# Performance work log

Hardware: AMD Instinct MI355X
Metric: run time of the kernel (lower is better)

The kernel has to match this reference:

```python
import jax, jax.numpy as jnp
import numpy as np

N_NODES = 100000
N_EDGES = 1600000
D = 128
BN_EPS = 1e-5

def setup_inputs() -> dict:
    key = jax.random.key(0)
    ks = jax.random.split(key, 6)
    h = jax.random.normal(ks[0], (N_NODES, D), dtype=jnp.float32)
    src = jax.random.randint(ks[1], (N_EDGES,), 0, N_NODES, dtype=jnp.int32)
    dst = jax.random.randint(ks[2], (N_EDGES,), 0, N_NODES, dtype=jnp.int32)
    eps = jnp.zeros((1,), dtype=jnp.float32)
    # 2-layer GIN apply_func MLP, scaled for stable activations
    W1 = jax.random.normal(ks[3], (D, D), dtype=jnp.float32) / np.sqrt(D)
    b1 = jnp.zeros((D,), dtype=jnp.float32)
    W2 = jax.random.normal(ks[4], (D, D), dtype=jnp.float32) / np.sqrt(D)
    b2 = jnp.zeros((D,), dtype=jnp.float32)
    gamma = jnp.ones((D,), dtype=jnp.float32)
    beta = jnp.zeros((D,), dtype=jnp.float32)
    return {"h": h, "src": src, "dst": dst, "eps": eps,
            "W1": W1, "b1": b1, "W2": W2, "b2": b2,
            "gamma": gamma, "beta": beta}

def reference(h, src, dst, eps, W1, b1, W2, b2, gamma, beta):
    # --- neighbor sum aggregation: update_all(copy_u('h'), fn.sum) ---
    msgs = h[src]                                   # [E, D] irregular gather
    neigh = jax.ops.segment_sum(msgs, dst, num_segments=N_NODES)  # [N, D]
    # --- eps-scaled self term ---
    x = (1.0 + eps[0]) * h + neigh                  # [N, D]
    # --- apply_func: 2-layer MLP ---
    x = jax.nn.relu(x @ W1 + b1)
    x = x @ W2 + b2
    # --- BatchNorm1d over node dim (training-mode batch stats) ---
    mean = jnp.mean(x, axis=0)
    var = jnp.mean(jnp.square(x - mean), axis=0)
    x = (x - mean) * jax.lax.rsqrt(var + BN_EPS) * gamma + beta
    # --- activation + residual ---
    x = jax.nn.relu(x)
    x = h + x  # residual (in_dim == out_dim)
    return x
```

## Files before the change

### kernel.cpp

```cpp
#include <hip/hip_runtime.h>

#define NN 100000
#define NE 1600000
#define DD 128
#define BN_EPS 1e-5f

#define SBSH 9
#define SBSZ 512
#define NSB ((NN + SBSZ - 1) / SBSZ)
#define CAPS 9216
#define EPB 8192
#define NBLK ((NE + EPB - 1) / EPB)
#define PREPBLKS 828
#define GRID_PS (NBLK + PREPBLKS)
#define TSZ 64
#define NTILE ((NN + TSZ - 1) / TSZ)
#define BN_BLOCKS 1024

typedef __attribute__((ext_vector_type(8))) short short8;
typedef __attribute__((ext_vector_type(4))) float floatx4;

__device__ __forceinline__ unsigned short f2bf(float f) {
    union { float f; unsigned u; } v; v.f = f;
    return (unsigned short)((v.u + 0x7FFFu + ((v.u >> 16) & 1u)) >> 16);
}
__device__ __forceinline__ float bf2f(unsigned short u) {
    union { unsigned u; float f; } v; v.u = ((unsigned)u) << 16;
    return v.f;
}

__global__ __launch_bounds__(256) void prep_scatter_kernel(
    const float* __restrict__ W1, const float* __restrict__ W2,
    unsigned short* __restrict__ W1t, unsigned short* __restrict__ W2t,
    const float* __restrict__ h, unsigned short* __restrict__ hb, int do_hb,
    const int* __restrict__ src, const int* __restrict__ dst,
    int* __restrict__ scnt, int* __restrict__ sbuf)
{
    __shared__ int bins[256];
    __shared__ int lofs[256];
    __shared__ int gbase[256];
    __shared__ int stmp[256];
    __shared__ int sorted[EPB];
    int t = threadIdx.x;

    if (blockIdx.x < NBLK) {
        bins[t] = 0;
        __syncthreads();
        int base = blockIdx.x * EPB;
        int ecnt = min(EPB, NE - base);
        for (int i = t; i < ecnt; i += 256)
            atomicAdd(&bins[dst[base + i] >> SBSH], 1);
        __syncthreads();
        int c = bins[t];
        stmp[t] = c;
        __syncthreads();
#pragma unroll
        for (int ofs = 1; ofs < 256; ofs <<= 1) {
            int u = (t >= ofs) ? stmp[t - ofs] : 0;
            __syncthreads();
            stmp[t] += u;
            __syncthreads();
        }
        int excl = stmp[t] - c;
        lofs[t] = excl;
        int gb = (t < NSB && c) ? atomicAdd(&scnt[t], c) : 0;
        gbase[t] = t * CAPS + gb;
        bins[t] = excl;
        __syncthreads();

        for (int i = t; i < ecnt; i += 256) {
            int d = dst[base + i];
            int p = atomicAdd(&bins[d >> SBSH], 1);
            sorted[p] = (src[base + i] << SBSH) | (d & (SBSZ - 1));
        }
        __syncthreads();

        for (int sb = t; sb < NSB; sb += 256) {
            int lb = lofs[sb], le = bins[sb];
            int g = gbase[sb];
            for (int j = lb; j < le; ++j)
                sbuf[g + (j - lb)] = sorted[j];
        }
    } else {
        int tid0 = (blockIdx.x - NBLK) * 256 + t;
        int stride = PREPBLKS * 256;
        for (int i = tid0; i < DD * DD; i += stride) {
            int n = i >> 7, k = i & 127;
            W1t[i] = f2bf(W1[k * DD + n]);
            W2t[i] = f2bf(W2[k * DD + n]);
        }
        if (do_hb) {
            const float4* h4 = (const float4*)h;
            ushort4* hb4 = (ushort4*)hb;
            for (int i = tid0; i < NN * (DD / 4); i += stride) {
                float4 v = h4[i];
                ushort4 o;
                o.x = f2bf(v.x); o.y = f2bf(v.y); o.z = f2bf(v.z); o.w = f2bf(v.w);
                hb4[i] = o;
            }
        }
    }
}

__global__ __launch_bounds__(512) void permute_kernel(
    const int* __restrict__ scnt, int* __restrict__ sbuf,
    int2* __restrict__ off2)
{
    __shared__ int ew[CAPS];
    __shared__ int cnt[SBSZ];
    __shared__ int beg[SBSZ];
    __shared__ int cur[SBSZ];
    __shared__ int stmp[512];
    int sb = blockIdx.x, t = threadIdx.x;
    cnt[t] = 0;
    __syncthreads();
    int n = min(scnt[sb], CAPS);
    int sbase = sb * CAPS;
    for (int i = t; i < n; i += 512) {
        int e = sbuf[sbase + i];
        ew[i] = e;
        atomicAdd(&cnt[e & (SBSZ - 1)], 1);
    }
    __syncthreads();
    int c = cnt[t];
    stmp[t] = c;
    __syncthreads();
#pragma unroll
    for (int ofs = 1; ofs < 512; ofs <<= 1) {
        int u = (t >= ofs) ? stmp[t - ofs] : 0;
        __syncthreads();
        stmp[t] += u;
        __syncthreads();
    }
    int excl = stmp[t] - c;
    beg[t] = excl;
    cur[t] = excl;
    off2[sb * SBSZ + t] = make_int2(sbase + excl, sbase + excl + c);
    __syncthreads();
    for (int i = t; i < n; i += 512) {
        int e = ew[i];
        int p = atomicAdd(&cur[e & (SBSZ - 1)], 1);
        sbuf[sbase + p] = e >> SBSH;
    }
}

template <bool HB>
__global__ __launch_bounds__(256) void gather_mlp_kernel(
    const float* __restrict__ h, const unsigned short* __restrict__ hb,
    const float* __restrict__ eps, const int2* __restrict__ off2,
    const int* __restrict__ srcs,
    const unsigned short* __restrict__ W1t, const unsigned short* __restrict__ W2t,
    const float* __restrict__ b1, const float* __restrict__ b2,
    unsigned short* __restrict__ Y, float* __restrict__ stats)
{
    __shared__ __align__(16) unsigned short xl[TSZ * 136];
    __shared__ __align__(16) char un[17408];

    int* beg64 = (int*)un;
    int* cnt64 = (int*)(un + 256);
    int* dh    = (int*)(un + 512);
    int* dcur  = (int*)(un + 768);
    unsigned char* order = (unsigned char*)(un + 1024);
    unsigned short* wl = (unsigned short*)un;
    float* sred = (float*)un;
    float* qred = sred + 2048;

    const int b = blockIdx.x;
    const int t = threadIdx.x;
    const int lane = t & 63;
    const int wv = t >> 6;
    const int m = lane & 15;
    const int hi = lane >> 4;

    if (t < 64) dh[t] = 0;
    __syncthreads();
    if (t < 64) {
        int2 oo = off2[b * TSZ + t];
        beg64[t] = oo.x;
        cnt64[t] = oo.y - oo.x;
        atomicAdd(&dh[min(cnt64[t], 63)], 1);
    }
    __syncthreads();
    if (t < 64) dcur[t] = dh[t];
    __syncthreads();
#pragma unroll
    for (int ofs = 1; ofs < 64; ofs <<= 1) {
        int u = (t < 64 && t >= ofs) ? dcur[t - ofs] : 0;
        __syncthreads();
        if (t < 64) dcur[t] += u;
        __syncthreads();
    }
    if (t < 64) dcur[t] -= dh[t];
    __syncthreads();
    if (t < 64) {
        int p = atomicAdd(&dcur[min(cnt64[t], 63)], 1);
        order[p] = (unsigned char)t;
    }
    __syncthreads();

    const float sE = 1.0f + eps[0];
    const float4* h4 = (const float4*)h;
    const short8* hb8 = (const short8*)hb;
    const int c8 = t & 15;
#pragma unroll
    for (int pass = 0; pass < 4; ++pass) {
        int nl = order[pass * 16 + (t >> 4)];
        int node = b * TSZ + nl;
        if (node >= NN) {
            short8 z = {0, 0, 0, 0, 0, 0, 0, 0};
            *(short8*)&xl[nl * 136 + c8 * 8] = z;
            continue;
        }
        float4 a0 = h4[node * 32 + c8 * 2];
        float4 a1 = h4[node * 32 + c8 * 2 + 1];
        float acc[8] = {sE * a0.x, sE * a0.y, sE * a0.z, sE * a0.w,
                        sE * a1.x, sE * a1.y, sE * a1.z, sE * a1.w};
        int e = beg64[nl], eend = beg64[nl] + cnt64[nl];
        if (HB) {
            for (; e + 3 < eend; e += 4) {
                int s0 = srcs[e], s1 = srcs[e + 1], s2 = srcs[e + 2], s3 = srcs[e + 3];
                short8 v0 = hb8[s0 * 16 + c8];
                short8 v1 = hb8[s1 * 16 + c8];
                short8 v2 = hb8[s2 * 16 + c8];
                short8 v3 = hb8[s3 * 16 + c8];
#pragma unroll
                for (int j = 0; j < 8; ++j) {
                    float t0 = bf2f((unsigned short)v0[j]) + bf2f((unsigned short)v1[j]);
                    float t1 = bf2f((unsigned short)v2[j]) + bf2f((unsigned short)v3[j]);
                    acc[j] += t0 + t1;
                }
            }
            for (; e < eend; ++e) {
                short8 v0 = hb8[srcs[e] * 16 + c8];
#pragma unroll
                for (int j = 0; j < 8; ++j) acc[j] += bf2f((unsigned short)v0[j]);
            }
        } else {
            for (; e + 1 < eend; e += 2) {
                int s0 = srcs[e], s1 = srcs[e + 1];
                float4 u0 = h4[s0 * 32 + c8 * 2], u1 = h4[s0 * 32 + c8 * 2 + 1];
                float4 w0 = h4[s1 * 32 + c8 * 2], w1 = h4[s1 * 32 + c8 * 2 + 1];
                acc[0] += u0.x + w0.x; acc[1] += u0.y + w0.y;
                acc[2] += u0.z + w0.z; acc[3] += u0.w + w0.w;
                acc[4] += u1.x + w1.x; acc[5] += u1.y + w1.y;
                acc[6] += u1.z + w1.z; acc[7] += u1.w + w1.w;
            }
            if (e < eend) {
                int s0 = srcs[e];
                float4 u0 = h4[s0 * 32 + c8 * 2], u1 = h4[s0 * 32 + c8 * 2 + 1];
                acc[0] += u0.x; acc[1] += u0.y; acc[2] += u0.z; acc[3] += u0.w;
                acc[4] += u1.x; acc[5] += u1.y; acc[6] += u1.z; acc[7] += u1.w;
            }
        }
        short8 o;
#pragma unroll
        for (int j = 0; j < 8; ++j) o[j] = (short)f2bf(acc[j]);
        *(short8*)&xl[nl * 136 + c8 * 8] = o;
    }
    __syncthreads();

    floatx4 acc[8];
#pragma unroll
    for (int i = 0; i < 8; ++i) acc[i] = (floatx4){0.f, 0.f, 0.f, 0.f};
    const short8* W1t8 = (const short8*)W1t;
#pragma unroll
    for (int hh = 0; hh < 2; ++hh) {
#pragma unroll
        for (int l = 0; l < 4; ++l) {
            int idx = t + l * 256;
            int nr = idx >> 4, c = idx & 15;
            *(short8*)&wl[nr * 136 + c * 8] = W1t8[(hh * 64 + nr) * 16 + c];
        }
        __syncthreads();
#pragma unroll
        for (int kc = 0; kc < 4; ++kc) {
            short8 a = *(const short8*)&xl[(wv * 16 + m) * 136 + kc * 32 + hi * 8];
#pragma unroll
            for (int ntl = 0; ntl < 4; ++ntl) {
                short8 bb = *(const short8*)&wl[(ntl * 16 + m) * 136 + kc * 32 + hi * 8];
                acc[hh * 4 + ntl] =
                    __builtin_amdgcn_mfma_f32_16x16x32_bf16(a, bb, acc[hh * 4 + ntl], 0, 0, 0);
            }
        }
        __syncthreads();
    }
#pragma unroll
    for (int nt = 0; nt < 8; ++nt) {
        float bv = b1[nt * 16 + m];
#pragma unroll
        for (int r = 0; r < 4; ++r) {
            float v = fmaxf(acc[nt][r] + bv, 0.f);
            xl[(wv * 16 + hi * 4 + r) * 136 + nt * 16 + m] = f2bf(v);
        }
    }
    __syncthreads();

#pragma unroll
    for (int i = 0; i < 8; ++i) acc[i] = (floatx4){0.f, 0.f, 0.f, 0.f};
    const short8* W2t8 = (const short8*)W2t;
#pragma unroll
    for (int hh = 0; hh < 2; ++hh) {
#pragma unroll
        for (int l = 0; l < 4; ++l) {
            int idx = t + l * 256;
            int nr = idx >> 4, c = idx & 15;
            *(short8*)&wl[nr * 136 + c * 8] = W2t8[(hh * 64 + nr) * 16 + c];
        }
        __syncthreads();
#pragma unroll
        for (int kc = 0; kc < 4; ++kc) {
            short8 a = *(const short8*)&xl[(wv * 16 + m) * 136 + kc * 32 + hi * 8];
#pragma unroll
            for (int ntl = 0; ntl < 4; ++ntl) {
                short8 bb = *(const short8*)&wl[(ntl * 16 + m) * 136 + kc * 32 + hi * 8];
                acc[hh * 4 + ntl] =
                    __builtin_amdgcn_mfma_f32_16x16x32_bf16(a, bb, acc[hh * 4 + ntl], 0, 0, 0);
            }
        }
        __syncthreads();
    }

#pragma unroll
    for (int nt = 0; nt < 8; ++nt) {
        float bv = b2[nt * 16 + m];
        float ss = 0.f, qq = 0.f;
#pragma unroll
        for (int r = 0; r < 4; ++r) {
            int row = wv * 16 + hi * 4 + r;
            float v = acc[nt][r] + bv;
            xl[row * 136 + nt * 16 + m] = f2bf(v);
            if (b * TSZ + row < NN) { ss += v; qq += v * v; }
        }
        sred[(nt * 16 + m) * 16 + wv * 4 + hi] = ss;
        qred[(nt * 16 + m) * 16 + wv * 4 + hi] = qq;
    }
    __syncthreads();

#pragma unroll
    for (int l = 0; l < 4; ++l) {
        int idx = t + l * 256;
        int row = idx >> 4, c = idx & 15;
        int g = b * TSZ + row;
        if (g < NN)
            ((short8*)Y)[g * 16 + c] = *(const short8*)&xl[row * 136 + c * 8];
    }
    if (t < 128) {
        float s = 0.f, q = 0.f;
#pragma unroll
        for (int j = 0; j < 16; ++j) { s += sred[t * 16 + j]; q += qred[t * 16 + j]; }
        atomicAdd(&stats[t], s);
        atomicAdd(&stats[DD + t], q);
    }
}

__global__ __launch_bounds__(256) void bn_final_kernel(
    const unsigned short* __restrict__ Y, const float* __restrict__ h,
    const float* __restrict__ gamma, const float* __restrict__ beta,
    const float* __restrict__ stats, float* __restrict__ out)
{
    const float invN = 1.0f / (float)NN;
    int t0 = blockIdx.x * 256 + threadIdx.x;
    int c8 = t0 & 15;
    float sc[8], sh[8];
#pragma unroll
    for (int j = 0; j < 8; ++j) {
        int col = c8 * 8 + j;
        float mu = stats[col] * invN;
        float var = stats[DD + col] * invN - mu * mu;
        float s = rsqrtf(var + BN_EPS) * gamma[col];
        sc[j] = s;
        sh[j] = beta[col] - mu * s;
    }
    const short8* Y8 = (const short8*)Y;
    const float4* H4 = (const float4*)h;
    float4* O4 = (float4*)out;
    const int total = NN * 16;
    const int stride = BN_BLOCKS * 256;
    for (int i = t0; i < total; i += stride) {
        short8 u = Y8[i];
        float4 h0 = H4[2 * i], h1 = H4[2 * i + 1];
        float4 r0, r1;
        r0.x = h0.x + fmaxf(bf2f((unsigned short)u[0]) * sc[0] + sh[0], 0.f);
        r0.y = h0.y + fmaxf(bf2f((unsigned short)u[1]) * sc[1] + sh[1], 0.f);
        r0.z = h0.z + fmaxf(bf2f((unsigned short)u[2]) * sc[2] + sh[2], 0.f);
        r0.w = h0.w + fmaxf(bf2f((unsigned short)u[3]) * sc[3] + sh[3], 0.f);
        r1.x = h1.x + fmaxf(bf2f((unsigned short)u[4]) * sc[4] + sh[4], 0.f);
        r1.y = h1.y + fmaxf(bf2f((unsigned short)u[5]) * sc[5] + sh[5], 0.f);
        r1.z = h1.z + fmaxf(bf2f((unsigned short)u[6]) * sc[6] + sh[6], 0.f);
        r1.w = h1.w + fmaxf(bf2f((unsigned short)u[7]) * sc[7] + sh[7], 0.f);
        O4[2 * i] = r0;
        O4[2 * i + 1] = r1;
    }
}

extern "C" void kernel_launch(void* const* d_in, const int* in_sizes, int n_in,
                              void* d_out, int out_size, void* d_ws, size_t ws_size,
                              hipStream_t stream)
{
    const float* h     = (const float*)d_in[0];
    const int*   src   = (const int*)d_in[1];
    const int*   dst   = (const int*)d_in[2];
    const float* eps   = (const float*)d_in[3];
    const float* W1    = (const float*)d_in[4];
    const float* b1    = (const float*)d_in[5];
    const float* W2    = (const float*)d_in[6];
    const float* b2    = (const float*)d_in[7];
    const float* gamma = (const float*)d_in[8];
    const float* beta  = (const float*)d_in[9];
    float* out = (float*)d_out;

    char* w = (char*)d_ws;
    size_t o = 0;
    float* stats    = (float*)(w + o); o += 256 * 4;
    int* scnt       = (int*)(w + o); o += 256 * 4;
    unsigned short* W1t = (unsigned short*)(w + o); o += (size_t)DD * DD * 2;
    unsigned short* W2t = (unsigned short*)(w + o); o += (size_t)DD * DD * 2;
    int2* off2      = (int2*)(w + o); o += (size_t)NSB * SBSZ * 8;
    int* sbuf       = (int*)(w + o); o += (size_t)NSB * CAPS * 4;
    unsigned short* xb  = (unsigned short*)(w + o); o += (size_t)NN * DD * 2;
    unsigned short* hb  = (unsigned short*)(w + o); o += (size_t)NN * DD * 2;
    const int use_hb = (ws_size >= o) ? 1 : 0;

    hipMemsetAsync(stats, 0, 512 * sizeof(int), stream);

    prep_scatter_kernel<<<GRID_PS, 256, 0, stream>>>(
        W1, W2, W1t, W2t, h, hb, use_hb, src, dst, scnt, sbuf);

    permute_kernel<<<NSB, 512, 0, stream>>>(scnt, sbuf, off2);

    if (use_hb)
        gather_mlp_kernel<true><<<NTILE, 256, 0, stream>>>(
            h, hb, eps, off2, sbuf, W1t, W2t, b1, b2, xb, stats);
    else
        gather_mlp_kernel<false><<<NTILE, 256, 0, stream>>>(
            h, hb, eps, off2, sbuf, W1t, W2t, b1, b2, xb, stats);

    bn_final_kernel<<<BN_BLOCKS, 256, 0, stream>>>(xb, h, gamma, beta, stats, out);
}
```

Measured before the change: 287.2 us.

## Load MFMA weight operands from global directly and simplify edge binning scatter

The MLP kernel no longer stages W1/W2 tiles through shared memory. Each lane now reads its bf16 weight fragments directly from global/L2, which removes the staging syncthreads and shrinks LDS to raise occupancy. The cost is repeated global weight reads per wave. The prep scatter drops the local shared-memory sort and writes edges straight to the global superbucket slots via shared atomics, at the cost of less coalesced writes. BN partial sums are now reduced with wave shuffles before going to shared memory.

```diff
diff --git a/kernel.cpp b/kernel.cpp
--- a/kernel.cpp
+++ b/kernel.cpp
@@ -37,10 +37,6 @@
     int* __restrict__ scnt, int* __restrict__ sbuf)
 {
     __shared__ int bins[256];
-    __shared__ int lofs[256];
-    __shared__ int gbase[256];
-    __shared__ int stmp[256];
-    __shared__ int sorted[EPB];
     int t = threadIdx.x;
 
     if (blockIdx.x < NBLK) {
@@ -52,34 +48,14 @@
             atomicAdd(&bins[dst[base + i] >> SBSH], 1);
         __syncthreads();
         int c = bins[t];
-        stmp[t] = c;
-        __syncthreads();
-#pragma unroll
-        for (int ofs = 1; ofs < 256; ofs <<= 1) {
-            int u = (t >= ofs) ? stmp[t - ofs] : 0;
-            __syncthreads();
-            stmp[t] += u;
-            __syncthreads();
-        }
-        int excl = stmp[t] - c;
-        lofs[t] = excl;
         int gb = (t < NSB && c) ? atomicAdd(&scnt[t], c) : 0;
-        gbase[t] = t * CAPS + gb;
-        bins[t] = excl;
-        __syncthreads();
-
+        __syncthreads();
+        bins[t] = t * CAPS + gb;
+        __syncthreads();
         for (int i = t; i < ecnt; i += 256) {
             int d = dst[base + i];
             int p = atomicAdd(&bins[d >> SBSH], 1);
-            sorted[p] = (src[base + i] << SBSH) | (d & (SBSZ - 1));
-        }
-        __syncthreads();
-
-        for (int sb = t; sb < NSB; sb += 256) {
-            int lb = lofs[sb], le = bins[sb];
-            int g = gbase[sb];
-            for (int j = lb; j < le; ++j)
-                sbuf[g + (j - lb)] = sorted[j];
+            sbuf[p] = (src[base + i] << SBSH) | (d & (SBSZ - 1));
         }
     } else {
         int tid0 = (blockIdx.x - NBLK) * 256 + t;
@@ -108,7 +84,6 @@
 {
     __shared__ int ew[CAPS];
     __shared__ int cnt[SBSZ];
-    __shared__ int beg[SBSZ];
     __shared__ int cur[SBSZ];
     __shared__ int stmp[512];
     int sb = blockIdx.x, t = threadIdx.x;
@@ -133,7 +108,6 @@
         __syncthreads();
     }
     int excl = stmp[t] - c;
-    beg[t] = excl;
     cur[t] = excl;
     off2[sb * SBSZ + t] = make_int2(sbase + excl, sbase + excl + c);
     __syncthreads();
@@ -154,16 +128,15 @@
     unsigned short* __restrict__ Y, float* __restrict__ stats)
 {
     __shared__ __align__(16) unsigned short xl[TSZ * 136];
-    __shared__ __align__(16) char un[17408];
+    __shared__ __align__(16) char un[4096];
 
     int* beg64 = (int*)un;
     int* cnt64 = (int*)(un + 256);
     int* dh    = (int*)(un + 512);
     int* dcur  = (int*)(un + 768);
     unsigned char* order = (unsigned char*)(un + 1024);
-    unsigned short* wl = (unsigned short*)un;
     float* sred = (float*)un;
-    float* qred = sred + 2048;
+    float* qred = sred + 512;
 
     const int b = blockIdx.x;
     const int t = threadIdx.x;
@@ -263,27 +236,15 @@
 #pragma unroll
     for (int i = 0; i < 8; ++i) acc[i] = (floatx4){0.f, 0.f, 0.f, 0.f};
     const short8* W1t8 = (const short8*)W1t;
-#pragma unroll
-    for (int hh = 0; hh < 2; ++hh) {
-#pragma unroll
-        for (int l = 0; l < 4; ++l) {
-            int idx = t + l * 256;
-            int nr = idx >> 4, c = idx & 15;
-            *(short8*)&wl[nr * 136 + c * 8] = W1t8[(hh * 64 + nr) * 16 + c];
-        }
-        __syncthreads();
-#pragma unroll
-        for (int kc = 0; kc < 4; ++kc) {
-            short8 a = *(const short8*)&xl[(wv * 16 + m) * 136 + kc * 32 + hi * 8];
-#pragma unroll
-            for (int ntl = 0; ntl < 4; ++ntl) {
-                short8 bb = *(const short8*)&wl[(ntl * 16 + m) * 136 + kc * 32 + hi * 8];
-                acc[hh * 4 + ntl] =
-                    __builtin_amdgcn_mfma_f32_16x16x32_bf16(a, bb, acc[hh * 4 + ntl], 0, 0, 0);
-            }
-        }
-        __syncthreads();
-    }
+    for (int kc = 0; kc < 4; ++kc) {
+        short8 a = *(const short8*)&xl[(wv * 16 + m) * 136 + kc * 32 + hi * 8];
+#pragma unroll
+        for (int nt = 0; nt < 8; ++nt) {
+            short8 bb = W1t8[(nt * 16 + m) * 16 + kc * 4 + hi];
+            acc[nt] = __builtin_amdgcn_mfma_f32_16x16x32_bf16(a, bb, acc[nt], 0, 0, 0);
+        }
+    }
+    __syncthreads();
 #pragma unroll
     for (int nt = 0; nt < 8; ++nt) {
         float bv = b1[nt * 16 + m];
@@ -298,27 +259,15 @@
 #pragma unroll
     for (int i = 0; i < 8; ++i) acc[i] = (floatx4){0.f, 0.f, 0.f, 0.f};
     const short8* W2t8 = (const short8*)W2t;
-#pragma unroll
-    for (int hh = 0; hh < 2; ++hh) {
-#pragma unroll
-        for (int l = 0; l < 4; ++l) {
-            int idx = t + l * 256;
-            int nr = idx >> 4, c = idx & 15;
-            *(short8*)&wl[nr * 136 + c * 8] = W2t8[(hh * 64 + nr) * 16 + c];
-        }
-        __syncthreads();
-#pragma unroll
-        for (int kc = 0; kc < 4; ++kc) {
-            short8 a = *(const short8*)&xl[(wv * 16 + m) * 136 + kc * 32 + hi * 8];
-#pragma unroll
-            for (int ntl = 0; ntl < 4; ++ntl) {
-                short8 bb = *(const short8*)&wl[(ntl * 16 + m) * 136 + kc * 32 + hi * 8];
-                acc[hh * 4 + ntl] =
-                    __builtin_amdgcn_mfma_f32_16x16x32_bf16(a, bb, acc[hh * 4 + ntl], 0, 0, 0);
-            }
-        }
-        __syncthreads();
-    }
+    for (int kc = 0; kc < 4; ++kc) {
+        short8 a = *(const short8*)&xl[(wv * 16 + m) * 136 + kc * 32 + hi * 8];
+#pragma unroll
+        for (int nt = 0; nt < 8; ++nt) {
+            short8 bb = W2t8[(nt * 16 + m) * 16 + kc * 4 + hi];
+            acc[nt] = __builtin_amdgcn_mfma_f32_16x16x32_bf16(a, bb, acc[nt], 0, 0, 0);
+        }
+    }
+    __syncthreads();
 
 #pragma unroll
     for (int nt = 0; nt < 8; ++nt) {
@@ -331,8 +280,14 @@
             xl[row * 136 + nt * 16 + m] = f2bf(v);
             if (b * TSZ + row < NN) { ss += v; qq += v * v; }
         }
-        sred[(nt * 16 + m) * 16 + wv * 4 + hi] = ss;
-        qred[(nt * 16 + m) * 16 + wv * 4 + hi] = qq;
+        ss += __shfl_xor(ss, 16, 64);
+        ss += __shfl_xor(ss, 32, 64);
+        qq += __shfl_xor(qq, 16, 64);
+        qq += __shfl_xor(qq, 32, 64);
+        if (hi == 0) {
+            sred[(nt * 16 + m) * 4 + wv] = ss;
+            qred[(nt * 16 + m) * 4 + wv] = qq;
+        }
     }
     __syncthreads();
 
@@ -345,9 +300,8 @@
             ((short8*)Y)[g * 16 + c] = *(const short8*)&xl[row * 136 + c * 8];
     }
     if (t < 128) {
-        float s = 0.f, q = 0.f;
-#pragma unroll
-        for (int j = 0; j < 16; ++j) { s += sred[t * 16 + j]; q += qred[t * 16 + j]; }
+        float s = sred[t * 4] + sred[t * 4 + 1] + sred[t * 4 + 2] + sred[t * 4 + 3];
+        float q = qred[t * 4] + qred[t * 4 + 1] + qred[t * 4 + 2] + qred[t * 4 + 3];
         atomicAdd(&stats[t], s);
         atomicAdd(&stats[DD + t], q);
     }
```

Result: slower. 326.3 us (+13.6%).
